# Kernel tuning notes

Measured on AMD Instinct MI355X. Metric: run time of the kernel, lower is better.

## Reference

```python
import jax, jax.numpy as jnp
import numpy as np

B, S, H, E, V = 32, 1024, 1024, 512, 32000
SCALE = 0.02


def setup_inputs() -> dict:
    key = jax.random.key(0)
    ks = jax.random.split(key, 16)
    inp = {
        "x": jax.random.randint(ks[0], (B, 1), 0, V),
        "hidden": jax.random.normal(ks[1], (1, B, H), jnp.float32),
        "cell": jax.random.normal(ks[2], (1, B, H), jnp.float32),
        "encoder_outputs": jax.random.normal(ks[3], (B, S, 2 * H), jnp.float32),
        # parameters
        "emb": jax.random.normal(ks[4], (V, E), jnp.float32) * SCALE,
        "attn_W": jax.random.normal(ks[5], (H, 3 * H), jnp.float32) * SCALE,
        "attn_b": jnp.zeros((H,), jnp.float32),
        "v_W": jax.random.normal(ks[6], (1, H), jnp.float32) * SCALE,
        "W_ih": jax.random.normal(ks[7], (4 * H, E + 2 * H), jnp.float32) * SCALE,
        "W_hh": jax.random.normal(ks[8], (4 * H, H), jnp.float32) * SCALE,
        "b_ih": jnp.zeros((4 * H,), jnp.float32),
        "b_hh": jnp.zeros((4 * H,), jnp.float32),
        "fc_W": jax.random.normal(ks[9], (V, H), jnp.float32) * SCALE,
        "fc_b": jnp.zeros((V,), jnp.float32),
    }
    # respect padding_idx=0: zero the padding embedding row
    inp["emb"] = inp["emb"].at[0].set(0.0)
    return inp


def reference(x, hidden, cell, encoder_outputs, emb, attn_W, attn_b, v_W,
              W_ih, W_hh, b_ih, b_hh, fc_W, fc_b):
    h = hidden[0]  # (B, H)
    c = cell[0]    # (B, H)

    # embedding lookup: (B, 1, E)
    embedded = emb[x]

    # Bahdanau additive attention
    src_len = encoder_outputs.shape[1]
    h_rep = jnp.broadcast_to(h[:, None, :], (h.shape[0], src_len, h.shape[1]))
    combined = jnp.concatenate([h_rep, encoder_outputs], axis=2)  # (B, S, 3H)
    energy = jnp.tanh(jnp.einsum('bsk,hk->bsh', combined, attn_W) + attn_b)
    scores = jnp.einsum('bsh,oh->bs', energy, v_W)  # (B, S), o == 1
    weights = jax.nn.softmax(scores, axis=1)
    context = jnp.einsum('bs,bsd->bd', weights, encoder_outputs)  # (B, 2H)

    # single-step LSTM cell (PyTorch gate order: i, f, g, o)
    lstm_in = jnp.concatenate([embedded[:, 0, :], context], axis=1)  # (B, E+2H)
    gates = lstm_in @ W_ih.T + b_ih + h @ W_hh.T + b_hh  # (B, 4H)
    i, f, g, o = jnp.split(gates, 4, axis=1)
    c_new = jax.nn.sigmoid(f) * c + jax.nn.sigmoid(i) * jnp.tanh(g)
    h_new = jax.nn.sigmoid(o) * jnp.tanh(c_new)

    prediction = (h_new @ fc_W.T + fc_b)[:, None, :]  # (B, 1, V)
    return prediction, h_new[None], c_new[None], weights
```

## Files before the change

kernel.cpp:

```cpp
#include <hip/hip_runtime.h>


typedef __attribute__((ext_vector_type(8))) short bf16x8;
typedef __attribute__((ext_vector_type(4))) float f32x4;

__device__ __forceinline__ unsigned short f2bf(float f) {
  unsigned int u = __float_as_uint(f);
  u += 0x7fffu + ((u >> 16) & 1u);
  return (unsigned short)(u >> 16);
}

__device__ __forceinline__ uint4 pack8(float4 a, float4 b) {
  union { unsigned short u[8]; uint4 v; } p;
  p.u[0] = f2bf(a.x); p.u[1] = f2bf(a.y); p.u[2] = f2bf(a.z); p.u[3] = f2bf(a.w);
  p.u[4] = f2bf(b.x); p.u[5] = f2bf(b.y); p.u[6] = f2bf(b.z); p.u[7] = f2bf(b.w);
  return p.v;
}

__global__ __launch_bounds__(256) void init_kernel(
    float* __restrict__ scores, float* __restrict__ gates, float* __restrict__ pred,
    float* __restrict__ lstm_in, const int* __restrict__ x, const float* __restrict__ emb,
    const float* __restrict__ b_ih, const float* __restrict__ b_hh,
    const float* __restrict__ fc_b)
{
  int idx = blockIdx.x * 256 + threadIdx.x;
  if (idx < 32768) { scores[idx] = 0.f; return; }
  idx -= 32768;
  if (idx < 131072) { gates[idx] = b_ih[idx & 4095] + b_hh[idx & 4095]; return; }
  idx -= 131072;
  if (idx < 1024000) { pred[idx] = fc_b[idx % 32000]; return; }
  idx -= 1024000;
  if (idx < 16384) {
    int b = idx >> 9, e = idx & 511;
    lstm_in[b * 2560 + e] = emb[(size_t)x[b] * 512 + e];
  }
}

__global__ __launch_bounds__(256) void hb_kernel(
    const float* __restrict__ hidden, const float* __restrict__ attn_W,
    const float* __restrict__ attn_b, float* __restrict__ hb)
{
  const int lane = threadIdx.x & 63;
  const int h = blockIdx.x * 4 + (threadIdx.x >> 6);
  const float4* wp = (const float4*)(attn_W + (size_t)h * 3072 + lane * 16);
  float4 w0 = wp[0], w1 = wp[1], w2 = wp[2], w3 = wp[3];
  float bias = attn_b[h];
  for (int b = 0; b < 32; ++b) {
    const float4* hp = (const float4*)(hidden + b * 1024 + lane * 16);
    float4 h0 = hp[0], h1 = hp[1], h2 = hp[2], h3 = hp[3];
    float p = w0.x*h0.x + w0.y*h0.y + w0.z*h0.z + w0.w*h0.w
            + w1.x*h1.x + w1.y*h1.y + w1.z*h1.z + w1.w*h1.w
            + w2.x*h2.x + w2.y*h2.y + w2.z*h2.z + w2.w*h2.w
            + w3.x*h3.x + w3.y*h3.y + w3.z*h3.z + w3.w*h3.w;
    #pragma unroll
    for (int d = 1; d < 64; d <<= 1) p += __shfl_xor(p, d);
    if (lane == 0) hb[b * 1024 + h] = p + bias;
  }
}

__global__ __launch_bounds__(256) void energy_kernel(
    const float* __restrict__ enc, const float* __restrict__ attn_W,
    const float* __restrict__ hb, const float* __restrict__ v_W,
    float* __restrict__ scores)
{
  __shared__ short Al[128][40];
  __shared__ short Bl[128][40];
  const int tid = threadIdx.x;
  const int lane = tid & 63, wave = tid >> 6;
  const int m0 = blockIdx.x * 128;
  const int n0 = blockIdx.y * 128;
  const int b  = m0 >> 10;
  const int wm = (wave >> 1) * 64, wn = (wave & 1) * 64;

  f32x4 acc[4][4];
  #pragma unroll
  for (int i = 0; i < 4; ++i)
    #pragma unroll
    for (int j = 0; j < 4; ++j) acc[i][j] = (f32x4){0.f, 0.f, 0.f, 0.f};

  const int srow = tid >> 1;
  const int scol = (tid & 1) * 16;
  const float* aptr = enc    + (size_t)(m0 + srow) * 2048 + scol;
  const float* bptr = attn_W + (size_t)(n0 + srow) * 3072 + 1024 + scol;

  const int fl = lane & 15, fq = (lane >> 4) * 8;

  for (int k0 = 0; k0 < 2048; k0 += 32) {
    const float4* a4 = (const float4*)(aptr + k0);
    float4 fa0 = a4[0], fa1 = a4[1], fa2 = a4[2], fa3 = a4[3];
    const float4* b4 = (const float4*)(bptr + k0);
    float4 fb0 = b4[0], fb1 = b4[1], fb2 = b4[2], fb3 = b4[3];
    *(uint4*)&Al[srow][scol]     = pack8(fa0, fa1);
    *(uint4*)&Al[srow][scol + 8] = pack8(fa2, fa3);
    *(uint4*)&Bl[srow][scol]     = pack8(fb0, fb1);
    *(uint4*)&Bl[srow][scol + 8] = pack8(fb2, fb3);
    __syncthreads();

    bf16x8 af[4], bf[4];
    #pragma unroll
    for (int i = 0; i < 4; ++i) af[i] = *(const bf16x8*)&Al[wm + i * 16 + fl][fq];
    #pragma unroll
    for (int j = 0; j < 4; ++j) bf[j] = *(const bf16x8*)&Bl[wn + j * 16 + fl][fq];
    #pragma unroll
    for (int i = 0; i < 4; ++i)
      #pragma unroll
      for (int j = 0; j < 4; ++j)
        acc[i][j] = __builtin_amdgcn_mfma_f32_16x16x32_bf16(af[i], bf[j], acc[i][j], 0, 0, 0);
    __syncthreads();
  }

  float rsum[4][4];
  #pragma unroll
  for (int i = 0; i < 4; ++i)
    #pragma unroll
    for (int r = 0; r < 4; ++r) rsum[i][r] = 0.f;

  const int col_base = n0 + wn + (lane & 15);
  #pragma unroll
  for (int j = 0; j < 4; ++j) {
    int col = col_base + j * 16;
    float hbv = hb[b * 1024 + col];
    float vv  = v_W[col];
    #pragma unroll
    for (int i = 0; i < 4; ++i)
      #pragma unroll
      for (int r = 0; r < 4; ++r)
        rsum[i][r] += vv * tanhf(acc[i][j][r] + hbv);
  }
  #pragma unroll
  for (int i = 0; i < 4; ++i)
    #pragma unroll
    for (int r = 0; r < 4; ++r) {
      float v = rsum[i][r];
      v += __shfl_xor(v, 1); v += __shfl_xor(v, 2);
      v += __shfl_xor(v, 4); v += __shfl_xor(v, 8);
      rsum[i][r] = v;
    }
  if ((lane & 15) == 0) {
    const int q = lane >> 4;
    const int sbase = (m0 & 1023) + wm;
    #pragma unroll
    for (int i = 0; i < 4; ++i)
      #pragma unroll
      for (int r = 0; r < 4; ++r)
        atomicAdd(&scores[b * 1024 + sbase + i * 16 + q * 4 + r], rsum[i][r]);
  }
}

__global__ __launch_bounds__(256) void softmax_kernel(
    const float* __restrict__ scores, float* __restrict__ wout)
{
  __shared__ float red[8];
  const int b = blockIdx.x, tid = threadIdx.x;
  const int lane = tid & 63, wave = tid >> 6;
  float v[4];
  #pragma unroll
  for (int r = 0; r < 4; ++r) v[r] = scores[b * 1024 + r * 256 + tid];
  float m = fmaxf(fmaxf(v[0], v[1]), fmaxf(v[2], v[3]));
  #pragma unroll
  for (int d = 1; d < 64; d <<= 1) m = fmaxf(m, __shfl_xor(m, d));
  if (lane == 0) red[wave] = m;
  __syncthreads();
  float M = fmaxf(fmaxf(red[0], red[1]), fmaxf(red[2], red[3]));
  float s = 0.f;
  #pragma unroll
  for (int r = 0; r < 4; ++r) { v[r] = expf(v[r] - M); s += v[r]; }
  #pragma unroll
  for (int d = 1; d < 64; d <<= 1) s += __shfl_xor(s, d);
  __syncthreads();
  if (lane == 0) red[4 + wave] = s;
  __syncthreads();
  float inv = 1.f / (red[4] + red[5] + red[6] + red[7]);
  #pragma unroll
  for (int r = 0; r < 4; ++r) wout[b * 1024 + r * 256 + tid] = v[r] * inv;
}

__global__ __launch_bounds__(256) void context_kernel(
    const float* __restrict__ enc, const float* __restrict__ wts, float* __restrict__ lstm_in)
{
  __shared__ float wl[1024];
  const int tid = threadIdx.x;
  const int b = blockIdx.y;
  const int col = blockIdx.x * 256 + tid;
  #pragma unroll
  for (int r = 0; r < 4; ++r) wl[r * 256 + tid] = wts[b * 1024 + r * 256 + tid];
  __syncthreads();
  const float* ep = enc + (size_t)b * (1024 * 2048) + col;
  float a0 = 0.f, a1 = 0.f, a2 = 0.f, a3 = 0.f;
  for (int s = 0; s < 1024; s += 8) {
    a0 += wl[s + 0] * ep[(size_t)(s + 0) * 2048];
    a1 += wl[s + 1] * ep[(size_t)(s + 1) * 2048];
    a2 += wl[s + 2] * ep[(size_t)(s + 2) * 2048];
    a3 += wl[s + 3] * ep[(size_t)(s + 3) * 2048];
    a0 += wl[s + 4] * ep[(size_t)(s + 4) * 2048];
    a1 += wl[s + 5] * ep[(size_t)(s + 5) * 2048];
    a2 += wl[s + 6] * ep[(size_t)(s + 6) * 2048];
    a3 += wl[s + 7] * ep[(size_t)(s + 7) * 2048];
  }
  lstm_in[b * 2560 + 512 + col] = (a0 + a1) + (a2 + a3);
}

__global__ __launch_bounds__(256) void skinny_gemm(
    const float* __restrict__ W, const float* __restrict__ X, float* __restrict__ out,
    int K, int Kc, int ldx, int ldo)
{
  __shared__ float Wl[256][33];
  const int tid = threadIdx.x;
  const int j0 = blockIdx.x * 256;
  const int k0 = blockIdx.y * Kc;
  float acc[32];
  #pragma unroll
  for (int b = 0; b < 32; ++b) acc[b] = 0.f;

  for (int kc = k0; kc < k0 + Kc; kc += 32) {
    __syncthreads();
    #pragma unroll
    for (int q = 0; q < 8; ++q) {
      int row = q * 32 + (tid >> 3);
      int col = (tid & 7) * 4;
      float4 v = *(const float4*)(W + (size_t)(j0 + row) * K + kc + col);
      Wl[row][col + 0] = v.x; Wl[row][col + 1] = v.y;
      Wl[row][col + 2] = v.z; Wl[row][col + 3] = v.w;
    }
    __syncthreads();
    float wreg[32];
    #pragma unroll
    for (int q = 0; q < 32; ++q) wreg[q] = Wl[tid][q];
    #pragma unroll
    for (int b = 0; b < 32; ++b) {
      const float* xp = X + b * ldx + kc;
      float s = 0.f;
      #pragma unroll
      for (int q = 0; q < 32; ++q) s += wreg[q] * xp[q];
      acc[b] += s;
    }
  }
  const int j = j0 + tid;
  #pragma unroll
  for (int b = 0; b < 32; ++b) atomicAdd(&out[(size_t)b * ldo + j], acc[b]);
}

__global__ __launch_bounds__(256) void cell_kernel(
    const float* __restrict__ gates, const float* __restrict__ cell_in,
    float* __restrict__ out_h, float* __restrict__ out_c)
{
  const int idx = blockIdx.x * 256 + threadIdx.x;
  const int b = idx >> 10, h = idx & 1023;
  const float* g = gates + b * 4096;
  float ig = g[h], fg = g[1024 + h], gg = g[2048 + h], og = g[3072 + h];
  float c = cell_in[idx];
  float si = 1.f / (1.f + expf(-ig));
  float sf = 1.f / (1.f + expf(-fg));
  float so = 1.f / (1.f + expf(-og));
  float cn = sf * c + si * tanhf(gg);
  float hn = so * tanhf(cn);
  out_c[idx] = cn;
  out_h[idx] = hn;
}

extern "C" void kernel_launch(void* const* d_in, const int* in_sizes, int n_in,
                              void* d_out, int out_size, void* d_ws, size_t ws_size,
                              hipStream_t stream) {
  const int*   x       = (const int*)  d_in[0];
  const float* hidden  = (const float*)d_in[1];
  const float* cell    = (const float*)d_in[2];
  const float* enc     = (const float*)d_in[3];
  const float* emb     = (const float*)d_in[4];
  const float* attn_W  = (const float*)d_in[5];
  const float* attn_b  = (const float*)d_in[6];
  const float* v_W     = (const float*)d_in[7];
  const float* W_ih    = (const float*)d_in[8];
  const float* W_hh    = (const float*)d_in[9];
  const float* b_ih    = (const float*)d_in[10];
  const float* b_hh    = (const float*)d_in[11];
  const float* fc_W    = (const float*)d_in[12];
  const float* fc_b    = (const float*)d_in[13];

  float* out   = (float*)d_out;
  float* pred  = out;
  float* out_h = out + 1024000;
  float* out_c = out + 1056768;
  float* out_w = out + 1089536;

  float* ws      = (float*)d_ws;
  float* scores  = ws;
  float* hb      = ws + 32768;
  float* lstm_in = ws + 65536;
  float* gates   = ws + 147456;

  init_kernel<<<4704, 256, 0, stream>>>(scores, gates, pred, lstm_in, x, emb, b_ih, b_hh, fc_b);
  hb_kernel<<<256, 256, 0, stream>>>(hidden, attn_W, attn_b, hb);
  energy_kernel<<<dim3(256, 8), 256, 0, stream>>>(enc, attn_W, hb, v_W, scores);
  softmax_kernel<<<32, 256, 0, stream>>>(scores, out_w);
  context_kernel<<<dim3(8, 32), 256, 0, stream>>>(enc, out_w, lstm_in);
  skinny_gemm<<<dim3(16, 16), 256, 0, stream>>>(W_ih, lstm_in, gates, 2560, 160, 2560, 4096);
  skinny_gemm<<<dim3(16, 8), 256, 0, stream>>>(W_hh, hidden, gates, 1024, 128, 1024, 4096);
  cell_kernel<<<128, 256, 0, stream>>>(gates, cell, out_h, out_c);
  skinny_gemm<<<dim3(125, 2), 256, 0, stream>>>(fc_W, out_h, pred, 1024, 512, 1024, 32000);
}
```

Before: 1.208 ms.

## Pre-convert encoder and attention weights to bf16 and stream via LDS-direct loads

A conversion pass writes encoder outputs and the relevant slice of attn_W to bf16 in workspace. A new energy kernel loads those tiles straight into swizzled LDS with global_load_lds and uses a K-step of 64. A new context kernel reads the bf16 copy, splits the sequence across blocks and accumulates with atomics. This removes the repeated fp32 reads and per-tile conversions in the energy GEMM and halves the bytes read by context, at the cost of an extra full pass over the 256MB encoder tensor plus a 128MB bf16 write. It also lowers context precision to bf16 and makes its sum order nondeterministic.

```diff
diff --git a/kernel.cpp b/kernel.cpp
--- a/kernel.cpp
+++ b/kernel.cpp
@@ -15,6 +15,14 @@
   p.u[0] = f2bf(a.x); p.u[1] = f2bf(a.y); p.u[2] = f2bf(a.z); p.u[3] = f2bf(a.w);
   p.u[4] = f2bf(b.x); p.u[5] = f2bf(b.y); p.u[6] = f2bf(b.z); p.u[7] = f2bf(b.w);
   return p.v;
+}
+
+__device__ __forceinline__ void gld16(const void* g, void* l) {
+  auto gp = reinterpret_cast<const __attribute__((address_space(1))) unsigned int*>(
+      reinterpret_cast<uintptr_t>(g));
+  auto lp = reinterpret_cast<__attribute__((address_space(3))) unsigned int*>(
+      reinterpret_cast<uintptr_t>(l));
+  __builtin_amdgcn_global_load_lds(gp, lp, 16, 0, 0);
 }
 
 __global__ __launch_bounds__(256) void init_kernel(
@@ -33,6 +41,29 @@
   if (idx < 16384) {
     int b = idx >> 9, e = idx & 511;
     lstm_in[b * 2560 + e] = emb[(size_t)x[b] * 512 + e];
+    return;
+  }
+  idx -= 16384;
+  if (idx < 65536) {
+    int b = idx >> 11, d = idx & 2047;
+    lstm_in[b * 2560 + 512 + d] = 0.f;
+  }
+}
+
+__global__ __launch_bounds__(256) void convert_kernel(
+    const float* __restrict__ enc, const float* __restrict__ attn_W,
+    short* __restrict__ Ac, short* __restrict__ Bc)
+{
+  if (blockIdx.x < 32768) {
+    size_t idx = (size_t)blockIdx.x * 256 + threadIdx.x;
+    const float4* p = (const float4*)enc + idx * 2;
+    float4 a = p[0], b = p[1];
+    *(uint4*)(Ac + idx * 8) = pack8(a, b);
+  } else {
+    int cc = (blockIdx.x - 32768) * 256 + threadIdx.x;
+    int r = cc >> 8, c8 = (cc & 255) * 8;
+    const float4* p = (const float4*)(attn_W + (size_t)r * 3072 + 1024 + c8);
+    *(uint4*)(Bc + (size_t)r * 2048 + c8) = pack8(p[0], p[1]);
   }
 }
 
@@ -58,6 +89,106 @@
   }
 }
 
+__global__ __launch_bounds__(256) void energy2_kernel(
+    const short* __restrict__ Ac, const short* __restrict__ Bc,
+    const float* __restrict__ hb, const float* __restrict__ v_W,
+    float* __restrict__ scores)
+{
+  __shared__ __align__(16) short Al[128 * 64];
+  __shared__ __align__(16) short Bl[128 * 64];
+  const int tid = threadIdx.x;
+  const int lane = tid & 63, wave = tid >> 6;
+  const int m0 = blockIdx.x * 128;
+  const int n0 = blockIdx.y * 128;
+  const int b  = m0 >> 10;
+  const int wm = (wave >> 1) * 64, wn = (wave & 1) * 64;
+
+  f32x4 acc[4][4];
+  #pragma unroll
+  for (int i = 0; i < 4; ++i)
+    #pragma unroll
+    for (int j = 0; j < 4; ++j) acc[i][j] = (f32x4){0.f, 0.f, 0.f, 0.f};
+
+  const short* ga[4]; const short* gb[4];
+  short* la[4]; short* lb[4];
+  #pragma unroll
+  for (int i = 0; i < 4; ++i) {
+    int L = i * 256 + tid;
+    int r = L >> 3, p = L & 7;
+    int kc = p ^ (r & 7);
+    ga[i] = Ac + (size_t)(m0 + r) * 2048 + kc * 8;
+    gb[i] = Bc + (size_t)(n0 + r) * 2048 + kc * 8;
+    la[i] = Al + (size_t)(i * 256 + (tid & ~63)) * 8;
+    lb[i] = Bl + (size_t)(i * 256 + (tid & ~63)) * 8;
+  }
+
+  const int fl = lane & 15, q = lane >> 4;
+
+  for (int k0 = 0; k0 < 2048; k0 += 64) {
+    #pragma unroll
+    for (int i = 0; i < 4; ++i) {
+      gld16(ga[i], la[i]);
+      gld16(gb[i], lb[i]);
+      ga[i] += 64; gb[i] += 64;
+    }
+    __syncthreads();
+    #pragma unroll
+    for (int s = 0; s < 2; ++s) {
+      bf16x8 af[4], bf[4];
+      const int c = s * 4 + q;
+      #pragma unroll
+      for (int i = 0; i < 4; ++i) {
+        int ra = wm + i * 16 + fl;
+        af[i] = *(const bf16x8*)&Al[ra * 64 + ((c ^ (ra & 7)) * 8)];
+        int rb = wn + i * 16 + fl;
+        bf[i] = *(const bf16x8*)&Bl[rb * 64 + ((c ^ (rb & 7)) * 8)];
+      }
+      #pragma unroll
+      for (int i = 0; i < 4; ++i)
+        #pragma unroll
+        for (int j = 0; j < 4; ++j)
+          acc[i][j] = __builtin_amdgcn_mfma_f32_16x16x32_bf16(af[i], bf[j], acc[i][j], 0, 0, 0);
+    }
+    __syncthreads();
+  }
+
+  float rsum[4][4];
+  #pragma unroll
+  for (int i = 0; i < 4; ++i)
+    #pragma unroll
+    for (int r = 0; r < 4; ++r) rsum[i][r] = 0.f;
+
+  const int col_base = n0 + wn + fl;
+  #pragma unroll
+  for (int j = 0; j < 4; ++j) {
+    int col = col_base + j * 16;
+    float hbv = hb[b * 1024 + col];
+    float vv  = v_W[col];
+    #pragma unroll
+    for (int i = 0; i < 4; ++i)
+      #pragma unroll
+      for (int r = 0; r < 4; ++r)
+        rsum[i][r] += vv * tanhf(acc[i][j][r] + hbv);
+  }
+  #pragma unroll
+  for (int i = 0; i < 4; ++i)
+    #pragma unroll
+    for (int r = 0; r < 4; ++r) {
+      float v = rsum[i][r];
+      v += __shfl_xor(v, 1); v += __shfl_xor(v, 2);
+      v += __shfl_xor(v, 4); v += __shfl_xor(v, 8);
+      rsum[i][r] = v;
+    }
+  if (fl == 0) {
+    const int sbase = (m0 & 1023) + wm;
+    #pragma unroll
+    for (int i = 0; i < 4; ++i)
+      #pragma unroll
+      for (int r = 0; r < 4; ++r)
+        atomicAdd(&scores[b * 1024 + sbase + i * 16 + q * 4 + r], rsum[i][r]);
+  }
+}
+
 __global__ __launch_bounds__(256) void energy_kernel(
     const float* __restrict__ enc, const float* __restrict__ attn_W,
     const float* __restrict__ hb, const float* __restrict__ v_W,
@@ -82,7 +213,6 @@
   const int scol = (tid & 1) * 16;
   const float* aptr = enc    + (size_t)(m0 + srow) * 2048 + scol;
   const float* bptr = attn_W + (size_t)(n0 + srow) * 3072 + 1024 + scol;
-
   const int fl = lane & 15, fq = (lane >> 4) * 8;
 
   for (int k0 = 0; k0 < 2048; k0 += 32) {
@@ -95,7 +225,6 @@
     *(uint4*)&Bl[srow][scol]     = pack8(fb0, fb1);
     *(uint4*)&Bl[srow][scol + 8] = pack8(fb2, fb3);
     __syncthreads();
-
     bf16x8 af[4], bf[4];
     #pragma unroll
     for (int i = 0; i < 4; ++i) af[i] = *(const bf16x8*)&Al[wm + i * 16 + fl][fq];
@@ -114,7 +243,6 @@
   for (int i = 0; i < 4; ++i)
     #pragma unroll
     for (int r = 0; r < 4; ++r) rsum[i][r] = 0.f;
-
   const int col_base = n0 + wn + (lane & 15);
   #pragma unroll
   for (int j = 0; j < 4; ++j) {
@@ -173,6 +301,36 @@
   float inv = 1.f / (red[4] + red[5] + red[6] + red[7]);
   #pragma unroll
   for (int r = 0; r < 4; ++r) wout[b * 1024 + r * 256 + tid] = v[r] * inv;
+}
+
+__global__ __launch_bounds__(256) void context2_kernel(
+    const short* __restrict__ Ac, const float* __restrict__ wts, float* __restrict__ lstm_in)
+{
+  __shared__ float wl[128];
+  const int tid = threadIdx.x;
+  const int b = blockIdx.y;
+  const int s0 = blockIdx.x * 128;
+  if (tid < 128) wl[tid] = wts[b * 1024 + s0 + tid];
+  __syncthreads();
+  const short* ep = Ac + (size_t)b * (1024 * 2048) + (size_t)s0 * 2048 + tid * 8;
+  float a[8];
+  #pragma unroll
+  for (int j = 0; j < 8; ++j) a[j] = 0.f;
+  for (int s = 0; s < 128; ++s) {
+    uint4 v = *(const uint4*)(ep + (size_t)s * 2048);
+    float w = wl[s];
+    a[0] += w * __uint_as_float(v.x << 16);
+    a[1] += w * __uint_as_float(v.x & 0xffff0000u);
+    a[2] += w * __uint_as_float(v.y << 16);
+    a[3] += w * __uint_as_float(v.y & 0xffff0000u);
+    a[4] += w * __uint_as_float(v.z << 16);
+    a[5] += w * __uint_as_float(v.z & 0xffff0000u);
+    a[6] += w * __uint_as_float(v.w << 16);
+    a[7] += w * __uint_as_float(v.w & 0xffff0000u);
+  }
+  float* dst = lstm_in + b * 2560 + 512 + tid * 8;
+  #pragma unroll
+  for (int j = 0; j < 8; ++j) atomicAdd(&dst[j], a[j]);
 }
 
 __global__ __launch_bounds__(256) void context_kernel(
@@ -287,12 +445,23 @@
   float* hb      = ws + 32768;
   float* lstm_in = ws + 65536;
   float* gates   = ws + 147456;
-
-  init_kernel<<<4704, 256, 0, stream>>>(scores, gates, pred, lstm_in, x, emb, b_ih, b_hh, fc_b);
+  short* Ac = (short*)((char*)d_ws + 1114112);
+  short* Bc = Ac + (size_t)32768 * 2048;
+  const size_t need = 1114112 + (size_t)32768 * 2048 * 2 + (size_t)1024 * 2048 * 2;
+  const bool fast = ws_size >= need;
+
+  init_kernel<<<4960, 256, 0, stream>>>(scores, gates, pred, lstm_in, x, emb, b_ih, b_hh, fc_b);
   hb_kernel<<<256, 256, 0, stream>>>(hidden, attn_W, attn_b, hb);
-  energy_kernel<<<dim3(256, 8), 256, 0, stream>>>(enc, attn_W, hb, v_W, scores);
-  softmax_kernel<<<32, 256, 0, stream>>>(scores, out_w);
-  context_kernel<<<dim3(8, 32), 256, 0, stream>>>(enc, out_w, lstm_in);
+  if (fast) {
+    convert_kernel<<<33792, 256, 0, stream>>>(enc, attn_W, Ac, Bc);
+    energy2_kernel<<<dim3(256, 8), 256, 0, stream>>>(Ac, Bc, hb, v_W, scores);
+    softmax_kernel<<<32, 256, 0, stream>>>(scores, out_w);
+    context2_kernel<<<dim3(8, 32), 256, 0, stream>>>(Ac, out_w, lstm_in);
+  } else {
+    energy_kernel<<<dim3(256, 8), 256, 0, stream>>>(enc, attn_W, hb, v_W, scores);
+    softmax_kernel<<<32, 256, 0, stream>>>(scores, out_w);
+    context_kernel<<<dim3(8, 32), 256, 0, stream>>>(enc, out_w, lstm_in);
+  }
   skinny_gemm<<<dim3(16, 16), 256, 0, stream>>>(W_ih, lstm_in, gates, 2560, 160, 2560, 4096);
   skinny_gemm<<<dim3(16, 8), 256, 0, stream>>>(W_hh, hidden, gates, 1024, 128, 1024, 4096);
   cell_kernel<<<128, 256, 0, stream>>>(gates, cell, out_h, out_c);
```

Result: faster. 1.060 ms (-12.3%).
